# Kernel tuning notes

Hardware: AMD Instinct MI355X
Metric: run time of the kernel (lower is better)

The kernel has to match this reference:

```python
import jax, jax.numpy as jnp
import numpy as np

B, C, H, W = 16, 512, 32, 32
MID = max(8, C // 4)      # gate hidden
CA_MID = max(8, C // 4)   # channel-attn hidden
LOW_RADIUS = 0.35


def dct_mat(N):
    # Orthonormal DCT-II matrix: D[k,n] = s_k * sqrt(2/N) * cos(pi*(2n+1)*k/(2N))
    k = jnp.arange(N, dtype=jnp.float32)[:, None]
    n = jnp.arange(N, dtype=jnp.float32)[None, :]
    M = jnp.cos(jnp.pi * (2.0 * n + 1.0) * k / (2.0 * N)) * jnp.sqrt(2.0 / N)
    return M.at[0].multiply(1.0 / jnp.sqrt(2.0))


def build_low_mask(Hh, Ww, low_radius):
    yy = jnp.arange(Hh, dtype=jnp.float32)[:, None] / max(Hh - 1, 1)
    xx = jnp.arange(Ww, dtype=jnp.float32)[None, :] / max(Ww - 1, 1)
    rr = jnp.sqrt(yy ** 2 + xx ** 2)
    rr = rr / jnp.maximum(rr.max(), 1e-6)
    return (rr <= low_radius).astype(jnp.float32)[None, None]  # [1,1,H,W]


def conv1x1(x, w, b):
    # x: [B,Cin,H,W], w: [Cout,Cin], b: [Cout]
    return jnp.einsum('bchw,oc->bohw', x, w) + b[None, :, None, None]


def freq_transform(x, gw1, gb1, gw2, gb2, Dh, Dw, lm):
    # gate: avgpool -> 1x1 -> relu -> 1x1 -> sigmoid, output 2 scalars per sample
    pooled = jnp.mean(x, axis=(2, 3), keepdims=True)  # [B,C,1,1]
    g = jax.nn.sigmoid(conv1x1(jax.nn.relu(conv1x1(pooled, gw1, gb1)), gw2, gb2))
    g_low, g_high = g[:, 0:1], g[:, 1:2]  # [B,1,1,1]
    # 2D ortho DCT: Dh @ x @ Dw^T
    freq = jnp.einsum('ih,bchw->bciw', Dh, x)
    freq = jnp.einsum('jw,bchw->bchj', Dw, freq)
    # frequency gating fused
    gated = freq * (g_low * lm + g_high * (1.0 - lm))
    # inverse: Dh^T @ freq @ Dw
    out = jnp.einsum('hi,bchw->bciw', Dh, gated)
    out = jnp.einsum('wj,bchw->bchj', Dw, out)
    return out


def setup_inputs() -> dict:
    key = jax.random.key(0)
    ks = jax.random.split(key, 24)
    s = 1.0 / np.sqrt(C)
    d = {
        'rgb': jax.random.normal(ks[0], (B, C, H, W), jnp.float32),
        'dsm': jax.random.normal(ks[1], (B, C, H, W), jnp.float32),
        'rgb_w': jax.random.normal(ks[2], (C, C), jnp.float32) * s,
        'rgb_b': jax.random.normal(ks[3], (C,), jnp.float32) * 0.01,
        'dsm_w': jax.random.normal(ks[4], (C, C), jnp.float32) * s,
        'dsm_b': jax.random.normal(ks[5], (C,), jnp.float32) * 0.01,
        'gate_w1': jax.random.normal(ks[6], (MID, C), jnp.float32) * s,
        'gate_b1': jax.random.normal(ks[7], (MID,), jnp.float32) * 0.01,
        'gate_w2': jax.random.normal(ks[8], (2, MID), jnp.float32) * (1.0 / np.sqrt(MID)),
        'gate_b2': jax.random.normal(ks[9], (2,), jnp.float32) * 0.01,
        'q_w': jax.random.normal(ks[10], (C, C), jnp.float32) * s,
        'q_b': jax.random.normal(ks[11], (C,), jnp.float32) * 0.01,
        'k_w': jax.random.normal(ks[12], (C, C), jnp.float32) * s,
        'k_b': jax.random.normal(ks[13], (C,), jnp.float32) * 0.01,
        'v_w': jax.random.normal(ks[14], (C, C), jnp.float32) * s,
        'v_b': jax.random.normal(ks[15], (C,), jnp.float32) * 0.01,
        'sp_w': jax.random.normal(ks[16], (C, C, 3, 3), jnp.float32) * (s / 3.0),
        'sp_b': jax.random.normal(ks[17], (C,), jnp.float32) * 0.01,
        'ca_w1': jax.random.normal(ks[18], (CA_MID, C), jnp.float32) * s,
        'ca_b1': jax.random.normal(ks[19], (CA_MID,), jnp.float32) * 0.01,
        'ca_w2': jax.random.normal(ks[20], (C, CA_MID), jnp.float32) * (1.0 / np.sqrt(CA_MID)),
        'ca_b2': jax.random.normal(ks[21], (C,), jnp.float32) * 0.01,
    }
    return d


def reference(rgb, dsm, rgb_w, rgb_b, dsm_w, dsm_b, gate_w1, gate_b1, gate_w2, gate_b2,
              q_w, q_b, k_w, k_b, v_w, v_b, sp_w, sp_b, ca_w1, ca_b1, ca_w2, ca_b2):
    Dh, Dw = dct_mat(H), dct_mat(W)
    lm = build_low_mask(H, W, LOW_RADIUS)

    rgb_p = conv1x1(rgb, rgb_w, rgb_b)
    dsm_p = conv1x1(dsm, dsm_w, dsm_b)

    rgb_f = freq_transform(rgb_p, gate_w1, gate_b1, gate_w2, gate_b2, Dh, Dw, lm)
    dsm_f = freq_transform(dsm_p, gate_w1, gate_b1, gate_w2, gate_b2, Dh, Dw, lm)

    q = conv1x1(rgb_f, q_w, q_b).reshape(B, C, H * W)
    k = conv1x1(dsm_f, k_w, k_b).reshape(B, C, H * W)
    v = conv1x1(dsm_f, v_w, v_b).reshape(B, C, H * W)

    # attn over spatial tokens: [B,N,N]
    scores = jnp.einsum('bcn,bcm->bnm', q, k) / jnp.sqrt(jnp.float32(C))
    attn = jax.nn.softmax(scores, axis=-1)
    out = jnp.einsum('bnm,bcm->bcn', attn, v).reshape(B, C, H, W)

    spatial = jax.lax.conv_general_dilated(
        out, sp_w, window_strides=(1, 1), padding='SAME',
        dimension_numbers=('NCHW', 'OIHW', 'NCHW')) + sp_b[None, :, None, None]

    pooled = jnp.mean(spatial, axis=(2, 3), keepdims=True)
    weight = jax.nn.sigmoid(conv1x1(jax.nn.relu(conv1x1(pooled, ca_w1, ca_b1)), ca_w2, ca_b2))
    return rgb_p + spatial * weight
```

## Files before the change

kernel.cpp:

```cpp
#include <hip/hip_runtime.h>

typedef long long i64;
typedef unsigned int u32;
typedef unsigned short u16;

#define Bq 16
#define Cq 512
#define Hq 32
#define Wq 32
#define Nq 1024
#define MIDq 128
#define XPBq 591872

typedef __attribute__((ext_vector_type(8))) short bf16x8;
typedef __attribute__((ext_vector_type(4))) float f32x4;

static __device__ __forceinline__ u16 f2bf(float f) {
  u32 u = __float_as_uint(f);
  u = (u + 0x7FFFu + ((u >> 16) & 1u)) >> 16;
  return (u16)u;
}
static __device__ __forceinline__ float bf2f(u16 h) {
  return __uint_as_float(((u32)h) << 16);
}

__global__ __launch_bounds__(256) void k_prep(
    const float* __restrict__ rgb_w, const float* __restrict__ dsm_w,
    const float* __restrict__ q_w, const float* __restrict__ k_w,
    const float* __restrict__ v_w, const float* __restrict__ sp_w,
    u16* __restrict__ rw_h, u16* __restrict__ rw_l,
    u16* __restrict__ dw_h, u16* __restrict__ dw_l,
    u16* __restrict__ qw_h, u16* __restrict__ qw_l,
    u16* __restrict__ kw_h, u16* __restrict__ kw_l,
    u16* __restrict__ vw_h, u16* __restrict__ vw_l,
    u16* __restrict__ w9h, u16* __restrict__ w9l,
    float* __restrict__ Dm, float* __restrict__ lm) {
  int blk = blockIdx.x, tid = threadIdx.x;
  if (blk < 1280) {
    int wi = blk >> 8;
    const float* src = wi == 0 ? rgb_w : wi == 1 ? dsm_w : wi == 2 ? q_w : wi == 3 ? k_w : v_w;
    u16* hi = wi == 0 ? rw_h : wi == 1 ? dw_h : wi == 2 ? qw_h : wi == 3 ? kw_h : vw_h;
    u16* lo = wi == 0 ? rw_l : wi == 1 ? dw_l : wi == 2 ? qw_l : wi == 3 ? kw_l : vw_l;
    i64 idx = ((i64)(blk & 255) * 256 + tid) * 4;
    float4 f = *(const float4*)(src + idx);
    ushort4 h, l;
    h.x = f2bf(f.x); l.x = f2bf(f.x - bf2f(h.x));
    h.y = f2bf(f.y); l.y = f2bf(f.y - bf2f(h.y));
    h.z = f2bf(f.z); l.z = f2bf(f.z - bf2f(h.z));
    h.w = f2bf(f.w); l.w = f2bf(f.w - bf2f(h.w));
    *(ushort4*)(hi + idx) = h;
    *(ushort4*)(lo + idx) = l;
  } else if (blk < 1536) {
    int idx = (blk - 1280) * 256 + tid;
    int o = idx >> 7;
    int c4 = (idx & 127) << 2;
    float vals[4][9];
#pragma unroll
    for (int j = 0; j < 4; j++) {
      const float* wp = sp_w + ((i64)o * Cq + c4 + j) * 9;
#pragma unroll
      for (int t = 0; t < 9; t++) vals[j][t] = wp[t];
    }
#pragma unroll
    for (int t = 0; t < 9; t++) {
      ushort4 h, l;
      h.x = f2bf(vals[0][t]); l.x = f2bf(vals[0][t] - bf2f(h.x));
      h.y = f2bf(vals[1][t]); l.y = f2bf(vals[1][t] - bf2f(h.y));
      h.z = f2bf(vals[2][t]); l.z = f2bf(vals[2][t] - bf2f(h.z));
      h.w = f2bf(vals[3][t]); l.w = f2bf(vals[3][t] - bf2f(h.w));
      i64 od = (i64)t * (Cq * Cq) + (i64)o * Cq + c4;
      *(ushort4*)(w9h + od) = h;
      *(ushort4*)(w9l + od) = l;
    }
  } else {
#pragma unroll
    for (int q4 = 0; q4 < 4; q4++) {
      int t = tid * 4 + q4;
      int i = t >> 5, j = t & 31;
      float v = cosf(3.14159265358979323846f * (2.0f * j + 1.0f) * (float)i / 64.0f) * 0.25f;
      if (i == 0) v *= 0.7071067811865476f;
      Dm[t] = v;
      float yy = i * (1.0f / 31.0f), xx = j * (1.0f / 31.0f);
      float rr = sqrtf(yy * yy + xx * xx) * 0.7071067811865476f;
      lm[t] = (rr <= 0.35f) ? 1.0f : 0.0f;
    }
  }
}

__global__ __launch_bounds__(64) void k_zero_border(u16* __restrict__ xp) {
  int i = blockIdx.x;
  int b = blockIdx.y;
  int arr = blockIdx.z;
  int pr;
  if (i < 34) pr = i;
  else if (i < 68) pr = 33 * 34 + (i - 34);
  else { int j = i - 68; pr = (1 + (j >> 1)) * 34 + (j & 1) * 33; }
  u16* p = xp + (i64)arr * ((i64)Bq * XPBq) + (i64)b * XPBq + (i64)pr * Cq;
  *(uint4*)(p + threadIdx.x * 8) = (uint4){0u, 0u, 0u, 0u};
}

__global__ __launch_bounds__(512) void k_gemm(
    const u16* __restrict__ Ahi, const u16* __restrict__ Alo,
    const float* __restrict__ Af32, int a_mode, i64 sAb,
    const u16* __restrict__ Bhi, const u16* __restrict__ Blo,
    const float* __restrict__ Bf32, int b_mode, i64 sBb,
    const float* __restrict__ bias, int bias_mode, float scale,
    int M, int N, int K,
    float* __restrict__ Cf, u16* __restrict__ Chi, u16* __restrict__ Clo,
    i64 sCb, int out_mode) {
  __shared__ __align__(16) u16 As_h[128][40];
  __shared__ __align__(16) u16 As_l[128][40];
  __shared__ __align__(16) u16 Bs_h[128][40];
  __shared__ __align__(16) u16 Bs_l[128][40];
  int tid = threadIdx.x;
  int gx = gridDim.x, gxy = gx * gridDim.y;
  int nwg = gxy * gridDim.z;
  int orig = blockIdx.x + gx * blockIdx.y + gxy * blockIdx.z;
  int wg = (nwg & 7) ? orig : ((orig & 7) * (nwg >> 3) + (orig >> 3));
  int b = wg / gxy;
  int rem = wg - b * gxy;
  int m0 = (rem / gx) << 7;
  int n0 = (rem - (rem / gx) * gx) << 7;
  const u16* pAhi = Ahi + (i64)b * (a_mode ? 0 : sAb);
  const u16* pAlo = Alo + (i64)b * (a_mode ? 0 : sAb);
  const float* pAf = a_mode ? (Af32 + (i64)b * sAb) : nullptr;
  const u16* pBhi = Bhi + (i64)b * (b_mode ? 0 : sBb);
  const u16* pBlo = Blo + (i64)b * (b_mode ? 0 : sBb);
  const float* pBf = b_mode ? (Bf32 + (i64)b * sBb) : nullptr;
  int lane = tid & 63;
  int wid = tid >> 6;
  int wm = (wid & 1) << 6;
  int wn = (wid >> 1) << 5;
  int l15 = lane & 15;
  int g8 = (lane >> 4) << 3;
  f32x4 acc[4][2];
#pragma unroll
  for (int mi = 0; mi < 4; mi++)
#pragma unroll
    for (int nj = 0; nj < 2; nj++)
      acc[mi][nj] = (f32x4){0.f, 0.f, 0.f, 0.f};

  for (int k0 = 0; k0 < K; k0 += 32) {
    if (a_mode == 0) {
      int r = tid >> 2, seg = tid & 3;
      *(uint4*)&As_h[r][seg * 8] = *(const uint4*)(pAhi + (i64)(m0 + r) * K + k0 + seg * 8);
      *(uint4*)&As_l[r][seg * 8] = *(const uint4*)(pAlo + (i64)(m0 + r) * K + k0 + seg * 8);
    } else {
      int cs = tid >> 6, ns = tid & 63;
      const float* src = pAf + (i64)(k0 + cs * 4) * M + m0 + ns * 2;
      float2 f[4];
#pragma unroll
      for (int j = 0; j < 4; j++) f[j] = *(const float2*)(src + (i64)j * M);
#pragma unroll
      for (int i = 0; i < 2; i++) {
        union { u16 u[4]; uint2 v; } hh, ll;
#pragma unroll
        for (int j = 0; j < 4; j++) {
          float x = i ? f[j].y : f[j].x;
          u16 h = f2bf(x);
          hh.u[j] = h;
          ll.u[j] = (u16)(__float_as_uint(x - bf2f(h)) >> 16);
        }
        *(uint2*)&As_h[2 * ns + i][cs * 4] = hh.v;
        *(uint2*)&As_l[2 * ns + i][cs * 4] = ll.v;
      }
    }
    if (b_mode == 0) {
      int r = tid >> 2, seg = tid & 3;
      *(uint4*)&Bs_h[r][seg * 8] = *(const uint4*)(pBhi + (i64)(n0 + r) * K + k0 + seg * 8);
      *(uint4*)&Bs_l[r][seg * 8] = *(const uint4*)(pBlo + (i64)(n0 + r) * K + k0 + seg * 8);
    } else {
      int cs = tid >> 6, ns = tid & 63;
      const float* src = pBf + (i64)(k0 + cs * 4) * N + n0 + ns * 2;
      float2 f[4];
#pragma unroll
      for (int j = 0; j < 4; j++) f[j] = *(const float2*)(src + (i64)j * N);
#pragma unroll
      for (int i = 0; i < 2; i++) {
        union { u16 u[4]; uint2 v; } hh, ll;
#pragma unroll
        for (int j = 0; j < 4; j++) {
          float x = i ? f[j].y : f[j].x;
          u16 h = f2bf(x);
          hh.u[j] = h;
          ll.u[j] = (u16)(__float_as_uint(x - bf2f(h)) >> 16);
        }
        *(uint2*)&Bs_h[2 * ns + i][cs * 4] = hh.v;
        *(uint2*)&Bs_l[2 * ns + i][cs * 4] = ll.v;
      }
    }
    __syncthreads();
    bf16x8 ah[4], al[4], bh[2], bl[2];
#pragma unroll
    for (int mi = 0; mi < 4; mi++) {
      int row = wm + mi * 16 + l15;
      ah[mi] = *(const bf16x8*)&As_h[row][g8];
      al[mi] = *(const bf16x8*)&As_l[row][g8];
    }
#pragma unroll
    for (int nj = 0; nj < 2; nj++) {
      int row = wn + nj * 16 + l15;
      bh[nj] = *(const bf16x8*)&Bs_h[row][g8];
      bl[nj] = *(const bf16x8*)&Bs_l[row][g8];
    }
#pragma unroll
    for (int mi = 0; mi < 4; mi++)
#pragma unroll
      for (int nj = 0; nj < 2; nj++) {
        acc[mi][nj] = __builtin_amdgcn_mfma_f32_16x16x32_bf16(ah[mi], bh[nj], acc[mi][nj], 0, 0, 0);
        acc[mi][nj] = __builtin_amdgcn_mfma_f32_16x16x32_bf16(ah[mi], bl[nj], acc[mi][nj], 0, 0, 0);
        acc[mi][nj] = __builtin_amdgcn_mfma_f32_16x16x32_bf16(al[mi], bh[nj], acc[mi][nj], 0, 0, 0);
      }
    __syncthreads();
  }

#pragma unroll
  for (int mi = 0; mi < 4; mi++)
#pragma unroll
    for (int nj = 0; nj < 2; nj++) {
      int col_g = n0 + wn + nj * 16 + l15;
      int row_b = m0 + wm + mi * 16 + ((lane >> 4) << 2);
      float v4[4];
#pragma unroll
      for (int r = 0; r < 4; r++) {
        float val = acc[mi][nj][r] * scale;
        if (bias_mode == 1) val += bias[row_b + r];
        else if (bias_mode == 2) val += bias[col_g];
        v4[r] = val;
      }
      if (out_mode == 0) {
#pragma unroll
        for (int r = 0; r < 4; r++)
          Cf[(i64)b * sCb + (i64)(row_b + r) * N + col_g] = v4[r];
      } else if (out_mode == 1) {
#pragma unroll
        for (int r = 0; r < 4; r++) {
          i64 o = (i64)b * sCb + (i64)(row_b + r) * N + col_g;
          u16 h = f2bf(v4[r]);
          Chi[o] = h;
          Clo[o] = f2bf(v4[r] - bf2f(h));
        }
      } else {
        int pr = ((col_g >> 5) + 1) * 34 + (col_g & 31) + 1;
        i64 o = (i64)b * sCb + (i64)pr * Cq + row_b;
        ushort4 hh, ll;
        hh.x = f2bf(v4[0]); ll.x = f2bf(v4[0] - bf2f(hh.x));
        hh.y = f2bf(v4[1]); ll.y = f2bf(v4[1] - bf2f(hh.y));
        hh.z = f2bf(v4[2]); ll.z = f2bf(v4[2] - bf2f(hh.z));
        hh.w = f2bf(v4[3]); ll.w = f2bf(v4[3] - bf2f(hh.w));
        *(ushort4*)(Chi + o) = hh;
        *(ushort4*)(Clo + o) = ll;
      }
    }
}

__global__ __launch_bounds__(512) void k_conv3_mfma(
    const u16* __restrict__ Wh, const u16* __restrict__ Wl,
    const u16* __restrict__ Xh, const u16* __restrict__ Xl,
    const float* __restrict__ bias, float* __restrict__ out) {
  __shared__ __align__(16) u16 As_h[128][40];
  __shared__ __align__(16) u16 As_l[128][40];
  __shared__ __align__(16) u16 Bs_h[204][40];
  __shared__ __align__(16) u16 Bs_l[204][40];
  int tid = threadIdx.x;
  int gx = gridDim.x, gxy = gx * gridDim.y;
  int nwg = gxy * gridDim.z;
  int orig = blockIdx.x + gx * blockIdx.y + gxy * blockIdx.z;
  int wg = (nwg & 7) ? orig : ((orig & 7) * (nwg >> 3) + (orig >> 3));
  int b = wg / gxy;
  int rem = wg - b * gxy;
  int m0 = (rem / gx) << 7;
  int n0 = (rem - (rem / gx) * gx) << 7;
  int lane = tid & 63;
  int wid = tid >> 6;
  int wm = (wid & 1) << 6;
  int wn = (wid >> 1) << 5;
  int l15 = lane & 15;
  int g8 = (lane >> 4) << 3;
  int yb = n0 >> 5;
  const u16* pXh = Xh + (i64)b * XPBq + (i64)(yb * 34) * Cq;
  const u16* pXl = Xl + (i64)b * XPBq + (i64)(yb * 34) * Cq;
  int bbase[2];
#pragma unroll
  for (int nj = 0; nj < 2; nj++) {
    int nloc = wn + nj * 16 + l15;
    bbase[nj] = (nloc >> 5) * 34 + (nloc & 31);
  }
  f32x4 acc[4][2];
#pragma unroll
  for (int mi = 0; mi < 4; mi++)
#pragma unroll
    for (int nj = 0; nj < 2; nj++)
      acc[mi][nj] = (f32x4){0.f, 0.f, 0.f, 0.f};

  for (int c0 = 0; c0 < Cq; c0 += 32) {
    for (int e = tid; e < 816; e += 512) {
      int row = e >> 2, q = e & 3;
      i64 src = (i64)row * Cq + c0 + q * 8;
      *(uint4*)&Bs_h[row][q * 8] = *(const uint4*)(pXh + src);
      *(uint4*)&Bs_l[row][q * 8] = *(const uint4*)(pXl + src);
    }
    for (int tap = 0; tap < 9; tap++) {
      int doff = (tap / 3) * 34 + (tap % 3);
      {
        int r = tid >> 2, seg = tid & 3;
        i64 wo = (i64)tap * (Cq * Cq) + (i64)(m0 + r) * Cq + c0 + seg * 8;
        *(uint4*)&As_h[r][seg * 8] = *(const uint4*)(Wh + wo);
        *(uint4*)&As_l[r][seg * 8] = *(const uint4*)(Wl + wo);
      }
      __syncthreads();
      bf16x8 ah[4], al[4], bh[2], bl[2];
#pragma unroll
      for (int mi = 0; mi < 4; mi++) {
        int row = wm + mi * 16 + l15;
        ah[mi] = *(const bf16x8*)&As_h[row][g8];
        al[mi] = *(const bf16x8*)&As_l[row][g8];
      }
#pragma unroll
      for (int nj = 0; nj < 2; nj++) {
        int row = bbase[nj] + doff;
        bh[nj] = *(const bf16x8*)&Bs_h[row][g8];
        bl[nj] = *(const bf16x8*)&Bs_l[row][g8];
      }
#pragma unroll
      for (int mi = 0; mi < 4; mi++)
#pragma unroll
        for (int nj = 0; nj < 2; nj++) {
          acc[mi][nj] = __builtin_amdgcn_mfma_f32_16x16x32_bf16(ah[mi], bh[nj], acc[mi][nj], 0, 0, 0);
          acc[mi][nj] = __builtin_amdgcn_mfma_f32_16x16x32_bf16(ah[mi], bl[nj], acc[mi][nj], 0, 0, 0);
          acc[mi][nj] = __builtin_amdgcn_mfma_f32_16x16x32_bf16(al[mi], bh[nj], acc[mi][nj], 0, 0, 0);
        }
      __syncthreads();
    }
  }

#pragma unroll
  for (int mi = 0; mi < 4; mi++)
#pragma unroll
    for (int nj = 0; nj < 2; nj++) {
      int col_g = n0 + wn + nj * 16 + l15;
#pragma unroll
      for (int r = 0; r < 4; r++) {
        int row_g = m0 + wm + mi * 16 + ((lane >> 4) << 2) + r;
        float val = acc[mi][nj][r] + bias[row_g];
        out[(i64)b * (Cq * Nq) + (i64)row_g * Nq + col_g] = val;
      }
    }
}

__global__ __launch_bounds__(256) void k_pool(const float* __restrict__ x, float* __restrict__ o) {
  int gw = (int)((blockIdx.x * 256 + threadIdx.x) >> 6);
  int ln = threadIdx.x & 63;
  const float* p = x + (i64)gw * Nq;
  float s = 0.f;
#pragma unroll
  for (int it = 0; it < 4; it++) {
    float4 v = *(const float4*)(p + ln * 4 + it * 256);
    s += v.x + v.y + v.z + v.w;
  }
#pragma unroll
  for (int off = 32; off > 0; off >>= 1) s += __shfl_xor(s, off, 64);
  if (ln == 0) o[gw] = s * (1.0f / 1024.0f);
}

__global__ __launch_bounds__(128) void k_gate(
    const float* __restrict__ pooled, const float* __restrict__ w1,
    const float* __restrict__ b1, const float* __restrict__ w2,
    const float* __restrict__ b2, float* __restrict__ g) {
  __shared__ float pl[Cq];
  __shared__ float h[MIDq];
  int bb = blockIdx.x, tid = threadIdx.x;
  for (int c = tid; c < Cq; c += 128) pl[c] = pooled[bb * Cq + c];
  __syncthreads();
  float s = b1[tid];
  const float* wr = w1 + (i64)tid * Cq;
  for (int c = 0; c < Cq; c++) s = fmaf(wr[c], pl[c], s);
  h[tid] = fmaxf(s, 0.f);
  __syncthreads();
  if (tid < 2) {
    float t = b2[tid];
    const float* w2r = w2 + tid * MIDq;
    for (int m = 0; m < MIDq; m++) t = fmaf(w2r[m], h[m], t);
    g[bb * 2 + tid] = 1.0f / (1.0f + expf(-t));
  }
}

__global__ __launch_bounds__(256) void k_freq(
    const float* __restrict__ xr, const float* __restrict__ xd,
    float* __restrict__ yr, float* __restrict__ yd,
    const float* __restrict__ g_r, const float* __restrict__ g_d,
    const float* __restrict__ Dm, const float* __restrict__ lm) {
  __shared__ float Ds[32][36], Dt[32][36], Xs[32][36], T1[32][36];
  int bid = blockIdx.x;
  const float* x; float* y; const float* g;
  if (bid < Bq * Cq) {
    x = xr + (i64)bid * Nq; y = yr + (i64)bid * Nq; g = g_r + (bid >> 9) * 2;
  } else {
    int id = bid - Bq * Cq;
    x = xd + (i64)id * Nq; y = yd + (i64)id * Nq; g = g_d + (id >> 9) * 2;
  }
  int tid = threadIdx.x;
  int r_ = tid >> 3, j4 = (tid & 7) << 2;
  {
    float4 dv = *(const float4*)(Dm + tid * 4);
    *(float4*)&Ds[r_][j4] = dv;
    Dt[j4 + 0][r_] = dv.x; Dt[j4 + 1][r_] = dv.y;
    Dt[j4 + 2][r_] = dv.z; Dt[j4 + 3][r_] = dv.w;
    *(float4*)&Xs[r_][j4] = *(const float4*)(x + tid * 4);
  }
  float gl = g[0], gh = g[1];
  __syncthreads();
  float a0 = 0, a1 = 0, a2 = 0, a3 = 0;
#pragma unroll
  for (int h = 0; h < 32; h++) {
    float a = Ds[r_][h];
    float4 bv = *(const float4*)&Xs[h][j4];
    a0 = fmaf(a, bv.x, a0); a1 = fmaf(a, bv.y, a1);
    a2 = fmaf(a, bv.z, a2); a3 = fmaf(a, bv.w, a3);
  }
  *(float4*)&T1[r_][j4] = make_float4(a0, a1, a2, a3);
  __syncthreads();
  a0 = a1 = a2 = a3 = 0;
#pragma unroll
  for (int w = 0; w < 32; w++) {
    float a = T1[r_][w];
    float4 bv = *(const float4*)&Dt[w][j4];
    a0 = fmaf(a, bv.x, a0); a1 = fmaf(a, bv.y, a1);
    a2 = fmaf(a, bv.z, a2); a3 = fmaf(a, bv.w, a3);
  }
  {
    float4 mv = *(const float4*)(lm + r_ * 32 + j4);
    a0 *= fmaf(gl, mv.x, gh * (1.f - mv.x));
    a1 *= fmaf(gl, mv.y, gh * (1.f - mv.y));
    a2 *= fmaf(gl, mv.z, gh * (1.f - mv.z));
    a3 *= fmaf(gl, mv.w, gh * (1.f - mv.w));
  }
  __syncthreads();
  *(float4*)&Xs[r_][j4] = make_float4(a0, a1, a2, a3);
  __syncthreads();
  a0 = a1 = a2 = a3 = 0;
#pragma unroll
  for (int ii = 0; ii < 32; ii++) {
    float a = Dt[r_][ii];
    float4 bv = *(const float4*)&Xs[ii][j4];
    a0 = fmaf(a, bv.x, a0); a1 = fmaf(a, bv.y, a1);
    a2 = fmaf(a, bv.z, a2); a3 = fmaf(a, bv.w, a3);
  }
  __syncthreads();
  *(float4*)&T1[r_][j4] = make_float4(a0, a1, a2, a3);
  __syncthreads();
  a0 = a1 = a2 = a3 = 0;
#pragma unroll
  for (int jj = 0; jj < 32; jj++) {
    float a = T1[r_][jj];
    float4 bv = *(const float4*)&Ds[jj][j4];
    a0 = fmaf(a, bv.x, a0); a1 = fmaf(a, bv.y, a1);
    a2 = fmaf(a, bv.z, a2); a3 = fmaf(a, bv.w, a3);
  }
  *(float4*)(y + tid * 4) = make_float4(a0, a1, a2, a3);
}

__global__ __launch_bounds__(256) void k_softmax_split(
    const float* __restrict__ sc, u16* __restrict__ ahi, u16* __restrict__ alo) {
  __shared__ float redm[4], reds[4];
  i64 row = blockIdx.x;
  const float* p = sc + row * (i64)Nq;
  int tid = threadIdx.x;
  float4 v = ((const float4*)p)[tid];
  float mx = fmaxf(fmaxf(v.x, v.y), fmaxf(v.z, v.w));
#pragma unroll
  for (int o = 32; o > 0; o >>= 1) mx = fmaxf(mx, __shfl_xor(mx, o, 64));
  if ((tid & 63) == 0) redm[tid >> 6] = mx;
  __syncthreads();
  mx = fmaxf(fmaxf(redm[0], redm[1]), fmaxf(redm[2], redm[3]));
  v.x = expf(v.x - mx); v.y = expf(v.y - mx);
  v.z = expf(v.z - mx); v.w = expf(v.w - mx);
  float s = v.x + v.y + v.z + v.w;
#pragma unroll
  for (int o = 32; o > 0; o >>= 1) s += __shfl_xor(s, o, 64);
  if ((tid & 63) == 0) reds[tid >> 6] = s;
  __syncthreads();
  s = reds[0] + reds[1] + reds[2] + reds[3];
  float inv = 1.0f / s;
  v.x *= inv; v.y *= inv; v.z *= inv; v.w *= inv;
  ushort4 h, l;
  h.x = f2bf(v.x); l.x = f2bf(v.x - bf2f(h.x));
  h.y = f2bf(v.y); l.y = f2bf(v.y - bf2f(h.y));
  h.z = f2bf(v.z); l.z = f2bf(v.z - bf2f(h.z));
  h.w = f2bf(v.w); l.w = f2bf(v.w - bf2f(h.w));
  *(ushort4*)(ahi + row * Nq + tid * 4) = h;
  *(ushort4*)(alo + row * Nq + tid * 4) = l;
}

__global__ __launch_bounds__(512) void k_ca(
    const float* __restrict__ pooled, const float* __restrict__ w1,
    const float* __restrict__ b1, const float* __restrict__ w2,
    const float* __restrict__ b2, float* __restrict__ wt) {
  __shared__ float pl[Cq];
  __shared__ float h[MIDq];
  int b = blockIdx.x, tid = threadIdx.x;
  pl[tid] = pooled[b * Cq + tid];
  __syncthreads();
  if (tid < MIDq) {
    float s = b1[tid];
    const float* wr = w1 + (i64)tid * Cq;
    for (int c = 0; c < Cq; c++) s = fmaf(wr[c], pl[c], s);
    h[tid] = fmaxf(s, 0.f);
  }
  __syncthreads();
  float s = b2[tid];
  const float* wr = w2 + (i64)tid * MIDq;
  for (int m = 0; m < MIDq; m++) s = fmaf(wr[m], h[m], s);
  wt[b * Cq + tid] = 1.0f / (1.0f + expf(-s));
}

__global__ __launch_bounds__(256) void k_final(
    const float* __restrict__ rgbp, const float* __restrict__ sp,
    const float* __restrict__ wt, float* __restrict__ out) {
  i64 idx = (i64)blockIdx.x * 256 + threadIdx.x;
  float4 a = ((const float4*)rgbp)[idx];
  float4 s = ((const float4*)sp)[idx];
  float w = wt[idx >> 8];
  float4 r;
  r.x = fmaf(s.x, w, a.x); r.y = fmaf(s.y, w, a.y);
  r.z = fmaf(s.z, w, a.z); r.w = fmaf(s.w, w, a.w);
  ((float4*)out)[idx] = r;
}

extern "C" void kernel_launch(void* const* d_in, const int* in_sizes, int n_in,
                              void* d_out, int out_size, void* d_ws, size_t ws_size,
                              hipStream_t stream) {
  (void)in_sizes; (void)n_in; (void)out_size; (void)ws_size;
  const float* rgb    = (const float*)d_in[0];
  const float* dsm    = (const float*)d_in[1];
  const float* rgb_w  = (const float*)d_in[2];
  const float* rgb_b  = (const float*)d_in[3];
  const float* dsm_w  = (const float*)d_in[4];
  const float* dsm_b  = (const float*)d_in[5];
  const float* gate_w1 = (const float*)d_in[6];
  const float* gate_b1 = (const float*)d_in[7];
  const float* gate_w2 = (const float*)d_in[8];
  const float* gate_b2 = (const float*)d_in[9];
  const float* q_w = (const float*)d_in[10];
  const float* q_b = (const float*)d_in[11];
  const float* k_w = (const float*)d_in[12];
  const float* k_b = (const float*)d_in[13];
  const float* v_w = (const float*)d_in[14];
  const float* v_b = (const float*)d_in[15];
  const float* sp_w = (const float*)d_in[16];
  const float* sp_b = (const float*)d_in[17];
  const float* ca_w1 = (const float*)d_in[18];
  const float* ca_b1 = (const float*)d_in[19];
  const float* ca_w2 = (const float*)d_in[20];
  const float* ca_b2 = (const float*)d_in[21];

  const i64 S  = (i64)Bq * Cq * Nq;
  const i64 SU = S;
  const i64 WE = (i64)Cq * Cq;
  const i64 XPT = (i64)Bq * XPBq;

  float* wsf = (float*)d_ws;
  float* rgbp   = wsf;
  float* dsmp   = wsf + S;
  float* rgbf   = wsf + 2 * S;
  float* dsmf   = wsf + 3 * S;
  float* scores  = dsmp;
  float* spatial = dsmf;
  u16* XPh = (u16*)dsmp;
  u16* XPl = XPh + XPT;
  float* smallr = wsf + 4 * S;
  float* Dm     = smallr;
  float* lm     = smallr + 1024;
  float* pooled = smallr + 2048;
  float* g_all  = smallr + 18432;
  float* wt     = smallr + 18496;
  u16* ub = (u16*)(wsf + 4 * S + 32768);
  u16* U0 = ub;          u16* U1 = ub + SU;
  u16* U2 = ub + 2 * SU;
  u16* U4 = ub + 4 * SU; u16* U5 = ub + 5 * SU;
  u16* wb = ub + 6 * SU;
  u16* rgbw_h = wb;           u16* rgbw_l = wb + WE;
  u16* dsmw_h = wb + 2 * WE;  u16* dsmw_l = wb + 3 * WE;
  u16* qw_h   = wb + 4 * WE;  u16* qw_l   = wb + 5 * WE;
  u16* kw_h   = wb + 6 * WE;  u16* kw_l   = wb + 7 * WE;
  u16* vw_h   = wb + 8 * WE;  u16* vw_l   = wb + 9 * WE;
  u16* w9h    = wb + 10 * WE; u16* w9l    = wb + 19 * WE;

  const i64 sT = (i64)Nq * Cq;
  const i64 sS = (i64)Nq * Nq;
  const float rsqc = 0.044194173824159216f;

  k_prep<<<1537, 256, 0, stream>>>(rgb_w, dsm_w, q_w, k_w, v_w, sp_w,
                                   rgbw_h, rgbw_l, dsmw_h, dsmw_l, qw_h, qw_l,
                                   kw_h, kw_l, vw_h, vw_l, w9h, w9l, Dm, lm);

  dim3 gW(Nq / 128, Cq / 128, Bq);
  dim3 gQ(Cq / 128, Nq / 128, Bq);
  dim3 gS(Nq / 128, Nq / 128, Bq);

  k_gemm<<<gW, 512, 0, stream>>>(rgbw_h, rgbw_l, nullptr, 0, 0,
                                 nullptr, nullptr, rgb, 1, sT,
                                 rgb_b, 1, 1.0f, Cq, Nq, Cq,
                                 rgbp, nullptr, nullptr, sT, 0);
  k_gemm<<<gW, 512, 0, stream>>>(dsmw_h, dsmw_l, nullptr, 0, 0,
                                 nullptr, nullptr, dsm, 1, sT,
                                 dsm_b, 1, 1.0f, Cq, Nq, Cq,
                                 dsmp, nullptr, nullptr, sT, 0);

  k_pool<<<(2 * Bq * Cq) / 4, 256, 0, stream>>>(rgbp, pooled);
  k_gate<<<32, 128, 0, stream>>>(pooled, gate_w1, gate_b1, gate_w2, gate_b2, g_all);

  k_freq<<<2 * Bq * Cq, 256, 0, stream>>>(rgbp, dsmp, rgbf, dsmf, g_all, g_all + 32, Dm, lm);

  k_gemm<<<gQ, 512, 0, stream>>>(nullptr, nullptr, rgbf, 1, sT,
                                 qw_h, qw_l, nullptr, 0, 0,
                                 q_b, 2, 1.0f, Nq, Cq, Cq,
                                 nullptr, U4, U5, sT, 1);
  k_gemm<<<gQ, 512, 0, stream>>>(nullptr, nullptr, dsmf, 1, sT,
                                 kw_h, kw_l, nullptr, 0, 0,
                                 k_b, 2, 1.0f, Nq, Cq, Cq,
                                 nullptr, U0, U1, sT, 1);
  k_gemm<<<gS, 512, 0, stream>>>(U4, U5, nullptr, 0, sT,
                                 U0, U1, nullptr, 0, sT,
                                 nullptr, 0, rsqc, Nq, Nq, Cq,
                                 scores, nullptr, nullptr, sS, 0);
  k_gemm<<<gW, 512, 0, stream>>>(vw_h, vw_l, nullptr, 0, 0,
                                 nullptr, nullptr, dsmf, 1, sT,
                                 v_b, 1, 1.0f, Cq, Nq, Cq,
                                 nullptr, U4, U5, sT, 1);
  k_softmax_split<<<Bq * Nq, 256, 0, stream>>>(scores, U0, U2);
  k_zero_border<<<dim3(132, Bq, 2), 64, 0, stream>>>(XPh);
  k_gemm<<<gW, 512, 0, stream>>>(U4, U5, nullptr, 0, sT,
                                 U0, U2, nullptr, 0, sS,
                                 nullptr, 0, 1.0f, Cq, Nq, Nq,
                                 nullptr, XPh, XPl, XPBq, 2);

  k_conv3_mfma<<<dim3(Nq / 128, Cq / 128, Bq), 512, 0, stream>>>(
      w9h, w9l, XPh, XPl, sp_b, spatial);

  k_pool<<<(Bq * Cq) / 4, 256, 0, stream>>>(spatial, pooled);
  k_ca<<<Bq, 512, 0, stream>>>(pooled, ca_w1, ca_b1, ca_w2, ca_b2, wt);

  k_final<<<(int)(S / 4 / 256), 256, 0, stream>>>(rgbp, spatial, wt, (float*)d_out);
}
```

Before: 727.9 us.

## Double-buffer conv3 weight tiles and prefetch inputs into registers

The 3x3 conv MFMA kernel now double-buffers the weight tile in shared memory. The next tap's weights, and the next channel chunk's input halo, are loaded from global into registers before the MFMAs run and written to LDS afterward. This cuts the per-tap sync count and hides global load latency behind compute. It also raises MFMA wave priority with s_setprio, at the cost of more LDS and more registers.

After: 731.8 us. About the same (+0.5%).

```diff
diff --git a/kernel.cpp b/kernel.cpp
--- a/kernel.cpp
+++ b/kernel.cpp
@@ -258,8 +258,8 @@
     const u16* __restrict__ Wh, const u16* __restrict__ Wl,
     const u16* __restrict__ Xh, const u16* __restrict__ Xl,
     const float* __restrict__ bias, float* __restrict__ out) {
-  __shared__ __align__(16) u16 As_h[128][40];
-  __shared__ __align__(16) u16 As_l[128][40];
+  __shared__ __align__(16) u16 As_h[2][128][40];
+  __shared__ __align__(16) u16 As_l[2][128][40];
   __shared__ __align__(16) u16 Bs_h[204][40];
   __shared__ __align__(16) u16 Bs_l[204][40];
   int tid = threadIdx.x;
@@ -286,6 +286,12 @@
     int nloc = wn + nj * 16 + l15;
     bbase[nj] = (nloc >> 5) * 34 + (nloc & 31);
   }
+  int ar = tid >> 2, aseg = tid & 3;
+  int b1row = tid >> 2, b1q = tid & 3;
+  int e2 = tid + 512;
+  int b2row = e2 >> 2, b2q = e2 & 3;
+  bool hasB2 = (e2 < 816);
+
   f32x4 acc[4][2];
 #pragma unroll
   for (int mi = 0; mi < 4; mi++)
@@ -293,28 +299,53 @@
     for (int nj = 0; nj < 2; nj++)
       acc[mi][nj] = (f32x4){0.f, 0.f, 0.f, 0.f};
 
+  {
+    i64 wo = (i64)(m0 + ar) * Cq + 0 + aseg * 8;
+    *(uint4*)&As_h[0][ar][aseg * 8] = *(const uint4*)(Wh + wo);
+    *(uint4*)&As_l[0][ar][aseg * 8] = *(const uint4*)(Wl + wo);
+    i64 s1 = (i64)b1row * Cq + b1q * 8;
+    *(uint4*)&Bs_h[b1row][b1q * 8] = *(const uint4*)(pXh + s1);
+    *(uint4*)&Bs_l[b1row][b1q * 8] = *(const uint4*)(pXl + s1);
+    if (hasB2) {
+      i64 s2 = (i64)b2row * Cq + b2q * 8;
+      *(uint4*)&Bs_h[b2row][b2q * 8] = *(const uint4*)(pXh + s2);
+      *(uint4*)&Bs_l[b2row][b2q * 8] = *(const uint4*)(pXl + s2);
+    }
+  }
+  __syncthreads();
+
+  int ph = 0;
   for (int c0 = 0; c0 < Cq; c0 += 32) {
-    for (int e = tid; e < 816; e += 512) {
-      int row = e >> 2, q = e & 3;
-      i64 src = (i64)row * Cq + c0 + q * 8;
-      *(uint4*)&Bs_h[row][q * 8] = *(const uint4*)(pXh + src);
-      *(uint4*)&Bs_l[row][q * 8] = *(const uint4*)(pXl + src);
-    }
-    for (int tap = 0; tap < 9; tap++) {
+    for (int tap = 0; tap < 9; tap++, ph++) {
+      int p = ph & 1;
+      bool morePh = (ph + 1 < 144);
+      uint4 pa_h, pa_l;
+      if (morePh) {
+        int ntap = (tap == 8) ? 0 : tap + 1;
+        int nc0  = (tap == 8) ? c0 + 32 : c0;
+        i64 wo = (i64)ntap * (Cq * Cq) + (i64)(m0 + ar) * Cq + nc0 + aseg * 8;
+        pa_h = *(const uint4*)(Wh + wo);
+        pa_l = *(const uint4*)(Wl + wo);
+      }
+      bool stageB = (tap == 8) && (c0 + 32 < Cq);
+      uint4 pb1h, pb1l, pb2h, pb2l;
+      if (stageB) {
+        i64 s1 = (i64)b1row * Cq + (c0 + 32) + b1q * 8;
+        pb1h = *(const uint4*)(pXh + s1);
+        pb1l = *(const uint4*)(pXl + s1);
+        if (hasB2) {
+          i64 s2 = (i64)b2row * Cq + (c0 + 32) + b2q * 8;
+          pb2h = *(const uint4*)(pXh + s2);
+          pb2l = *(const uint4*)(pXl + s2);
+        }
+      }
       int doff = (tap / 3) * 34 + (tap % 3);
-      {
-        int r = tid >> 2, seg = tid & 3;
-        i64 wo = (i64)tap * (Cq * Cq) + (i64)(m0 + r) * Cq + c0 + seg * 8;
-        *(uint4*)&As_h[r][seg * 8] = *(const uint4*)(Wh + wo);
-        *(uint4*)&As_l[r][seg * 8] = *(const uint4*)(Wl + wo);
-      }
-      __syncthreads();
       bf16x8 ah[4], al[4], bh[2], bl[2];
 #pragma unroll
       for (int mi = 0; mi < 4; mi++) {
         int row = wm + mi * 16 + l15;
-        ah[mi] = *(const bf16x8*)&As_h[row][g8];
-        al[mi] = *(const bf16x8*)&As_l[row][g8];
+        ah[mi] = *(const bf16x8*)&As_h[p][row][g8];
+        al[mi] = *(const bf16x8*)&As_l[p][row][g8];
       }
 #pragma unroll
       for (int nj = 0; nj < 2; nj++) {
@@ -322,6 +353,7 @@
         bh[nj] = *(const bf16x8*)&Bs_h[row][g8];
         bl[nj] = *(const bf16x8*)&Bs_l[row][g8];
       }
+      __builtin_amdgcn_s_setprio(1);
 #pragma unroll
       for (int mi = 0; mi < 4; mi++)
 #pragma unroll
@@ -330,6 +362,22 @@
           acc[mi][nj] = __builtin_amdgcn_mfma_f32_16x16x32_bf16(ah[mi], bl[nj], acc[mi][nj], 0, 0, 0);
           acc[mi][nj] = __builtin_amdgcn_mfma_f32_16x16x32_bf16(al[mi], bh[nj], acc[mi][nj], 0, 0, 0);
         }
+      __builtin_amdgcn_s_setprio(0);
+      if (morePh) {
+        *(uint4*)&As_h[p ^ 1][ar][aseg * 8] = pa_h;
+        *(uint4*)&As_l[p ^ 1][ar][aseg * 8] = pa_l;
+      }
+      if (tap == 8) {
+        __syncthreads();
+        if (stageB) {
+          *(uint4*)&Bs_h[b1row][b1q * 8] = pb1h;
+          *(uint4*)&Bs_l[b1row][b1q * 8] = pb1l;
+          if (hasB2) {
+            *(uint4*)&Bs_h[b2row][b2q * 8] = pb2h;
+            *(uint4*)&Bs_l[b2row][b2q * 8] = pb2l;
+          }
+        }
+      }
       __syncthreads();
     }
   }
```

## Switch 3x3 conv kernel to 32x32x16 MFMA with 4 waves of 64x64 tiles

Applied to the files above, without the earlier changes.

The 3x3 spatial conv kernel now uses 32x32x16 bf16 MFMA instructions instead of 16x16x32, and 4 waves per block instead of 8. Each wave covers a 64x64 output tile with 2x2 accumulators of 16 floats. Each wave loads fewer LDS fragments per MFMA, so operand reuse goes up and LDS traffic goes down. The cost is more accumulator registers per thread and fewer waves per block to hide load latency.

After: 724.6 us. Within noise of the previous version (-0.4%).

```diff
diff --git a/kernel.cpp b/kernel.cpp
--- a/kernel.cpp
+++ b/kernel.cpp
@@ -14,6 +14,7 @@
 
 typedef __attribute__((ext_vector_type(8))) short bf16x8;
 typedef __attribute__((ext_vector_type(4))) float f32x4;
+typedef __attribute__((ext_vector_type(16))) float f32x16;
 
 static __device__ __forceinline__ u16 f2bf(float f) {
   u32 u = __float_as_uint(f);
@@ -254,7 +255,7 @@
     }
 }
 
-__global__ __launch_bounds__(512) void k_conv3_mfma(
+__global__ __launch_bounds__(256) void k_conv3_mfma(
     const u16* __restrict__ Wh, const u16* __restrict__ Wl,
     const u16* __restrict__ Xh, const u16* __restrict__ Xl,
     const float* __restrict__ bias, float* __restrict__ out) {
@@ -274,27 +275,27 @@
   int lane = tid & 63;
   int wid = tid >> 6;
   int wm = (wid & 1) << 6;
-  int wn = (wid >> 1) << 5;
-  int l15 = lane & 15;
-  int g8 = (lane >> 4) << 3;
+  int wn = (wid >> 1) << 6;
+  int l31 = lane & 31;
+  int kg = (lane >> 5) << 3;
   int yb = n0 >> 5;
   const u16* pXh = Xh + (i64)b * XPBq + (i64)(yb * 34) * Cq;
   const u16* pXl = Xl + (i64)b * XPBq + (i64)(yb * 34) * Cq;
   int bbase[2];
 #pragma unroll
   for (int nj = 0; nj < 2; nj++) {
-    int nloc = wn + nj * 16 + l15;
+    int nloc = wn + nj * 32 + l31;
     bbase[nj] = (nloc >> 5) * 34 + (nloc & 31);
   }
-  f32x4 acc[4][2];
-#pragma unroll
-  for (int mi = 0; mi < 4; mi++)
+  f32x16 acc[2][2];
+#pragma unroll
+  for (int mi = 0; mi < 2; mi++)
 #pragma unroll
     for (int nj = 0; nj < 2; nj++)
-      acc[mi][nj] = (f32x4){0.f, 0.f, 0.f, 0.f};
+      acc[mi][nj] = (f32x16){0.f,0.f,0.f,0.f,0.f,0.f,0.f,0.f,0.f,0.f,0.f,0.f,0.f,0.f,0.f,0.f};
 
   for (int c0 = 0; c0 < Cq; c0 += 32) {
-    for (int e = tid; e < 816; e += 512) {
+    for (int e = tid; e < 816; e += 256) {
       int row = e >> 2, q = e & 3;
       i64 src = (i64)row * Cq + c0 + q * 8;
       *(uint4*)&Bs_h[row][q * 8] = *(const uint4*)(pXh + src);
@@ -303,47 +304,56 @@
     for (int tap = 0; tap < 9; tap++) {
       int doff = (tap / 3) * 34 + (tap % 3);
       {
-        int r = tid >> 2, seg = tid & 3;
-        i64 wo = (i64)tap * (Cq * Cq) + (i64)(m0 + r) * Cq + c0 + seg * 8;
-        *(uint4*)&As_h[r][seg * 8] = *(const uint4*)(Wh + wo);
-        *(uint4*)&As_l[r][seg * 8] = *(const uint4*)(Wl + wo);
+        int r = tid >> 1, q0 = (tid & 1) << 1;
+        i64 wo = (i64)tap * (Cq * Cq) + (i64)(m0 + r) * Cq + c0;
+        *(uint4*)&As_h[r][q0 * 8]       = *(const uint4*)(Wh + wo + q0 * 8);
+        *(uint4*)&As_h[r][(q0 + 1) * 8] = *(const uint4*)(Wh + wo + (q0 + 1) * 8);
+        *(uint4*)&As_l[r][q0 * 8]       = *(const uint4*)(Wl + wo + q0 * 8);
+        *(uint4*)&As_l[r][(q0 + 1) * 8] = *(const uint4*)(Wl + wo + (q0 + 1) * 8);
       }
       __syncthreads();
-      bf16x8 ah[4], al[4], bh[2], bl[2];
-#pragma unroll
-      for (int mi = 0; mi < 4; mi++) {
-        int row = wm + mi * 16 + l15;
-        ah[mi] = *(const bf16x8*)&As_h[row][g8];
-        al[mi] = *(const bf16x8*)&As_l[row][g8];
-      }
-#pragma unroll
-      for (int nj = 0; nj < 2; nj++) {
-        int row = bbase[nj] + doff;
-        bh[nj] = *(const bf16x8*)&Bs_h[row][g8];
-        bl[nj] = *(const bf16x8*)&Bs_l[row][g8];
-      }
-#pragma unroll
-      for (int mi = 0; mi < 4; mi++)
+#pragma unroll
+      for (int kstep = 0; kstep < 2; kstep++) {
+        int kc = kstep * 16 + kg;
+        bf16x8 ah[2], al[2], bh[2], bl[2];
+#pragma unroll
+        for (int mi = 0; mi < 2; mi++) {
+          int row = wm + mi * 32 + l31;
+          ah[mi] = *(const bf16x8*)&As_h[row][kc];
+          al[mi] = *(const bf16x8*)&As_l[row][kc];
+        }
 #pragma unroll
         for (int nj = 0; nj < 2; nj++) {
-          acc[mi][nj] = __builtin_amdgcn_mfma_f32_16x16x32_bf16(ah[mi], bh[nj], acc[mi][nj], 0, 0, 0);
-          acc[mi][nj] = __builtin_amdgcn_mfma_f32_16x16x32_bf16(ah[mi], bl[nj], acc[mi][nj], 0, 0, 0);
-          acc[mi][nj] = __builtin_amdgcn_mfma_f32_16x16x32_bf16(al[mi], bh[nj], acc[mi][nj], 0, 0, 0);
+          int row = bbase[nj] + doff;
+          bh[nj] = *(const bf16x8*)&Bs_h[row][kc];
+          bl[nj] = *(const bf16x8*)&Bs_l[row][kc];
         }
+#pragma unroll
+        for (int mi = 0; mi < 2; mi++)
+#pragma unroll
+          for (int nj = 0; nj < 2; nj++) {
+            acc[mi][nj] = __builtin_amdgcn_mfma_f32_32x32x16_bf16(ah[mi], bh[nj], acc[mi][nj], 0, 0, 0);
+            acc[mi][nj] = __builtin_amdgcn_mfma_f32_32x32x16_bf16(ah[mi], bl[nj], acc[mi][nj], 0, 0, 0);
+            acc[mi][nj] = __builtin_amdgcn_mfma_f32_32x32x16_bf16(al[mi], bh[nj], acc[mi][nj], 0, 0, 0);
+          }
+      }
       __syncthreads();
     }
   }
 
 #pragma unroll
-  for (int mi = 0; mi < 4; mi++)
+  for (int mi = 0; mi < 2; mi++)
 #pragma unroll
     for (int nj = 0; nj < 2; nj++) {
-      int col_g = n0 + wn + nj * 16 + l15;
-#pragma unroll
-      for (int r = 0; r < 4; r++) {
-        int row_g = m0 + wm + mi * 16 + ((lane >> 4) << 2) + r;
-        float val = acc[mi][nj][r] + bias[row_g];
-        out[(i64)b * (Cq * Nq) + (i64)row_g * Nq + col_g] = val;
+      int col_g = n0 + wn + nj * 32 + l31;
+#pragma unroll
+      for (int g = 0; g < 4; g++) {
+        int row_b = m0 + wm + mi * 32 + g * 8 + ((lane >> 5) << 2);
+#pragma unroll
+        for (int r = 0; r < 4; r++) {
+          float val = acc[mi][nj][g * 4 + r] + bias[row_b + r];
+          out[(i64)b * (Cq * Nq) + (i64)(row_b + r) * Nq + col_g] = val;
+        }
       }
     }
 }
@@ -635,7 +645,7 @@
                                  nullptr, 0, 1.0f, Cq, Nq, Nq,
                                  nullptr, XPh, XPl, XPBq, 2);
 
-  k_conv3_mfma<<<dim3(Nq / 128, Cq / 128, Bq), 512, 0, stream>>>(
+  k_conv3_mfma<<<dim3(Nq / 128, Cq / 128, Bq), 256, 0, stream>>>(
       w9h, w9l, XPh, XPl, sp_b, spatial);
 
   k_pool<<<(Bq * Cq) / 4, 256, 0, stream>>>(spatial, pooled);
```
